# Kernel optimization log

Hardware: AMD Instinct MI355X
Metric: run time of the kernel (lower is better)

The kernel has to match this reference:

```python
import jax, jax.numpy as jnp
import numpy as np

NUM_EMBEDDINGS = 1024
EMBEDDING_DIM = 256


def setup_inputs() -> dict:
    key = jax.random.key(0)
    kx, kc = jax.random.split(key)
    x = jax.random.normal(kx, (32, 256, 64, 64), dtype=jnp.float32)
    # codebook initialized uniform(-1/K, 1/K) as in the torch module
    codebook = jax.random.uniform(
        kc, (NUM_EMBEDDINGS, EMBEDDING_DIM), dtype=jnp.float32,
        minval=-1.0 / NUM_EMBEDDINGS, maxval=1.0 / NUM_EMBEDDINGS)
    return {"x": x, "codebook": codebook}


def reference(x, codebook):
    # x: (B, C, H, W) -> (B, H, W, C) -> (N, C)
    B, C, H, W = x.shape
    xf = jnp.transpose(x, (0, 2, 3, 1)).reshape(-1, C)  # (N, C)
    dist = (jnp.sum(xf * xf, axis=1, keepdims=True)
            + jnp.sum(codebook * codebook, axis=1)
            - 2.0 * jnp.matmul(xf, codebook.T))
    indices = jnp.argmin(dist, axis=1)[:, None]  # (N, 1), matches torch unsqueeze(1)
    quantized = codebook[indices[:, 0]].reshape(B, H, W, C)  # gather
    quantized = jnp.transpose(quantized, (0, 3, 1, 2))  # (B, C, H, W)
    return indices, quantized
```

## Files before the change

### kernel.cpp

```cpp
#include <hip/hip_runtime.h>
#include <stdint.h>

#define CDIM   256
#define KCODES 1024
#define HWSZ   4096
#define NROWS  131072
#define DELTA_P 4.7e-4f

#define WS_BQ    0
#define WS_IDX   4096
#define WS_CBBF  528384
#define WS_CNT   1052672
#define WS_LIST  1052800
#define WS_SLOT  1577216
#define WS_AS    2625792
#define WS_XC    3150080

typedef __attribute__((ext_vector_type(8))) short short8;
typedef __attribute__((ext_vector_type(4))) float f32x4;

__device__ inline unsigned short bf16rne(float f) {
    uint32_t u = __float_as_uint(f);
    u += 0x7FFF + ((u >> 16) & 1);
    return (unsigned short)(u >> 16);
}

__device__ __forceinline__ unsigned umin32(unsigned a, unsigned b) { return a < b ? a : b; }
__device__ __forceinline__ unsigned umax32(unsigned a, unsigned b) { return a > b ? a : b; }

__device__ __forceinline__ unsigned long long packkey(float s, int k) {
    unsigned b = __float_as_uint(s);
    unsigned m = (b & 0x80000000u) ? ~b : (b | 0x80000000u);
    return ((unsigned long long)m << 32) | (unsigned)k;
}

__global__ void codesq_kernel(const float* __restrict__ cb, float* __restrict__ Bq) {
#pragma clang fp contract(off)
    int k = blockIdx.x * 256 + threadIdx.x;
    if (k >= KCODES) return;
    const float* er = cb + (size_t)k * CDIM;
    float half_s[2];
    for (int h = 0; h < 2; ++h) {
        float r[8];
        #pragma unroll
        for (int j = 0; j < 8; ++j) { float v = er[h*128 + j]; r[j] = v * v; }
        for (int i = 8; i < 128; i += 8) {
            #pragma unroll
            for (int j = 0; j < 8; ++j) { float v = er[h*128 + i + j]; float sq = v*v; r[j] = r[j] + sq; }
        }
        half_s[h] = ((r[0]+r[1]) + (r[2]+r[3])) + ((r[4]+r[5]) + (r[6]+r[7]));
    }
    Bq[k] = half_s[0] + half_s[1];
}

__global__ void cbcvt_kernel(const float* __restrict__ cb, unsigned short* __restrict__ cbbf,
                             int* __restrict__ counter) {
    int i = blockIdx.x * 256 + threadIdx.x;
    float4 v = ((const float4*)cb)[i];
    ushort4 o;
    o.x = bf16rne(v.x); o.y = bf16rne(v.y); o.z = bf16rne(v.z); o.w = bf16rne(v.w);
    ((ushort4*)cbbf)[i] = o;
    if (i == 0) *counter = 0;
}

__global__ __launch_bounds__(256, 2)
void screen_kernel(const float* __restrict__ x, const unsigned short* __restrict__ cbbf,
                   const float* __restrict__ Bq,
                   int* __restrict__ idx_out, float* __restrict__ outF,
                   int* __restrict__ flag_list, int* __restrict__ counter,
                   unsigned long long* __restrict__ slots) {
    __shared__ unsigned short xs[64 * 264];
    __shared__ unsigned int sRed[4][64][2];

    const int t = threadIdx.x;
    const int w = t >> 6, l = t & 63;
    const int l15 = l & 15, quad = l >> 4;
    const int r0 = blockIdx.x * 64;
    const float* xbase = x + (size_t)(r0 >> 12) * (CDIM * HWSZ) + (r0 & 4095);

    {
        int cbase = (t >> 4) * 2;
        int row4  = (t & 15) * 4;
        for (int it = 0; it < 8; ++it) {
            int c = cbase + it * 32;
            float4 fa = *(const float4*)(xbase + (size_t)c * HWSZ + row4);
            float4 fb = *(const float4*)(xbase + (size_t)(c + 1) * HWSZ + row4);
            *(uint32_t*)&xs[(row4+0)*264 + c] = (uint32_t)bf16rne(fa.x) | ((uint32_t)bf16rne(fb.x) << 16);
            *(uint32_t*)&xs[(row4+1)*264 + c] = (uint32_t)bf16rne(fa.y) | ((uint32_t)bf16rne(fb.y) << 16);
            *(uint32_t*)&xs[(row4+2)*264 + c] = (uint32_t)bf16rne(fa.z) | ((uint32_t)bf16rne(fb.z) << 16);
            *(uint32_t*)&xs[(row4+3)*264 + c] = (uint32_t)bf16rne(fa.w) | ((uint32_t)bf16rne(fb.w) << 16);
        }
    }

    __syncthreads();

    short8 af[8][4];
    #pragma unroll
    for (int step = 0; step < 8; ++step)
        #pragma unroll
        for (int rf = 0; rf < 4; ++rf)
            af[step][rf] = *(const short8*)&xs[(rf*16 + l15)*264 + step*32 + quad*8];

    const unsigned short* bbase = cbbf + (size_t)(w*32 + l15) * CDIM + quad * 8;
    const int kbase = w*32 + l15;

    unsigned int K1[16], K2[16];
    #pragma unroll
    for (int i = 0; i < 16; ++i) { K1[i] = 0xFFFFFFFFu; K2[i] = 0xFFFFFFFFu; }

    for (int kt = 0; kt < 8; ++kt) {
        float bqp0 = Bq[kt*128 + kbase]      + 0.75f;
        float bqp1 = Bq[kt*128 + kbase + 16] + 0.75f;

        f32x4 acc[4][2];
        #pragma unroll
        for (int rf = 0; rf < 4; ++rf)
            #pragma unroll
            for (int cf = 0; cf < 2; ++cf) acc[rf][cf] = (f32x4){0.f, 0.f, 0.f, 0.f};

        #pragma unroll
        for (int step = 0; step < 8; ++step) {
            int koff = step * 32;
            short8 bfr0 = *(const short8*)(bbase + (size_t)(kt*128)      * CDIM + koff);
            short8 bfr1 = *(const short8*)(bbase + (size_t)(kt*128 + 16) * CDIM + koff);
            #pragma unroll
            for (int rf = 0; rf < 4; ++rf) {
                acc[rf][0] = __builtin_amdgcn_mfma_f32_16x16x32_bf16(af[step][rf], bfr0, acc[rf][0], 0, 0, 0);
                acc[rf][1] = __builtin_amdgcn_mfma_f32_16x16x32_bf16(af[step][rf], bfr1, acc[rf][1], 0, 0, 0);
            }
        }

        unsigned int kk0 = (unsigned)(kt*128 + kbase);
        unsigned int kk1 = kk0 + 16u;
        #pragma unroll
        for (int rf = 0; rf < 4; ++rf)
            #pragma unroll
            for (int reg = 0; reg < 4; ++reg) {
                int st = rf*4 + reg;
                {
                    float s = fmaf(-2.f, acc[rf][0][reg], bqp0);
                    unsigned int key = (__float_as_uint(s) & 0xFFFFFC00u) | kk0;
                    unsigned int t1 = umin32(key, K1[st]);
                    unsigned int t2 = umax32(key, K1[st]);
                    K1[st] = t1;
                    K2[st] = umin32(t2, K2[st]);
                }
                {
                    float s = fmaf(-2.f, acc[rf][1][reg], bqp1);
                    unsigned int key = (__float_as_uint(s) & 0xFFFFFC00u) | kk1;
                    unsigned int t1 = umin32(key, K1[st]);
                    unsigned int t2 = umax32(key, K1[st]);
                    K1[st] = t1;
                    K2[st] = umin32(t2, K2[st]);
                }
            }
    }

    #pragma unroll
    for (int st = 0; st < 16; ++st) {
        #pragma unroll
        for (int m = 1; m < 16; m <<= 1) {
            unsigned int o1 = (unsigned int)__shfl_xor((int)K1[st], m, 64);
            unsigned int o2 = (unsigned int)__shfl_xor((int)K2[st], m, 64);
            unsigned int n2 = umin32(umax32(K1[st], o1), umin32(K2[st], o2));
            K1[st] = umin32(K1[st], o1);
            K2[st] = n2;
        }
    }
    if (l15 == 0) {
        #pragma unroll
        for (int rf = 0; rf < 4; ++rf)
            #pragma unroll
            for (int reg = 0; reg < 4; ++reg) {
                int r = rf*16 + quad*4 + reg;
                int st = rf*4 + reg;
                sRed[w][r][0] = K1[st];
                sRed[w][r][1] = K2[st];
            }
    }
    __syncthreads();
    if (t < 64) {
        unsigned int A1 = sRed[0][t][0], A2 = sRed[0][t][1];
        #pragma unroll
        for (int ww = 1; ww < 4; ++ww) {
            unsigned int B1 = sRed[ww][t][0], B2 = sRed[ww][t][1];
            unsigned int n2 = umin32(umax32(A1, B1), umin32(A2, B2));
            A1 = umin32(A1, B1);
            A2 = n2;
        }
        int row = r0 + t;
        int k1i = (int)(A1 & 1023u);
        idx_out[row] = k1i;
        outF[row] = (float)k1i;
        float v1 = __uint_as_float(A1 & 0xFFFFFC00u);
        float v2 = __uint_as_float(A2 & 0xFFFFFC00u);
        if (!(v2 - v1 > DELTA_P)) {
            int pos = atomicAdd(counter, 1);
            flag_list[pos] = row;
            slots[pos] = 0xFFFFFFFFFFFFFFFFull;
        }
    }
}

__global__ __launch_bounds__(256)
void xcopy_kernel(const float* __restrict__ x, const int* __restrict__ flag_list,
                  const int* __restrict__ counter, float* __restrict__ xc, int capn) {
    int cnt = *counter; if (cnt > capn) cnt = capn;
    for (int base = blockIdx.x * 64; base < cnt; base += gridDim.x * 64) {
        int j = base + (threadIdx.x >> 2);
        if (j < cnt) {
            int row = flag_list[j];
            const float* xr = x + (size_t)(row >> 12) * (CDIM * HWSZ) + (row & 4095);
            int c0 = (threadIdx.x & 3) * 64;
            float* dst = xc + (size_t)j * CDIM + c0;
            #pragma unroll 8
            for (int c = 0; c < 64; ++c)
                dst[c] = xr[(size_t)(c0 + c) * HWSZ];
        }
    }
}

__global__ void asq_kernel(const float* __restrict__ x, const float* __restrict__ xc,
                           const int* __restrict__ flag_list, const int* __restrict__ counter,
                           float* __restrict__ As, int capn) {
#pragma clang fp contract(off)
    int cnt = *counter;
    int jf = blockIdx.x * 256 + threadIdx.x;
    if (jf >= cnt) return;
    const float* src;
    size_t stride;
    if (jf < capn) { src = xc + (size_t)jf * CDIM; stride = 1; }
    else {
        int row = flag_list[jf];
        src = x + (size_t)(row >> 12) * (CDIM * HWSZ) + (row & 4095);
        stride = HWSZ;
    }
    float half_s[2];
    for (int h = 0; h < 2; ++h) {
        float r[8];
        #pragma unroll
        for (int j = 0; j < 8; ++j) { float v = src[(size_t)(h*128 + j) * stride]; r[j] = v * v; }
        for (int i = 8; i < 128; i += 8) {
            #pragma unroll
            for (int j = 0; j < 8; ++j) { float v = src[(size_t)(h*128 + i + j) * stride]; float sq = v*v; r[j] = r[j] + sq; }
        }
        half_s[h] = ((r[0]+r[1]) + (r[2]+r[3])) + ((r[4]+r[5]) + (r[6]+r[7]));
    }
    As[jf] = half_s[0] + half_s[1];
}

__global__ __launch_bounds__(256, 2)
void rescore_kernel(const float* __restrict__ x, const float* __restrict__ cb,
                    const float* __restrict__ Bq,
                    const int* __restrict__ flag_list, const int* __restrict__ counter,
                    const float* __restrict__ xc, const float* __restrict__ As, int capn,
                    unsigned long long* __restrict__ slots) {
    __shared__ float cbs[64 * 256];

    int cnt = *counter;
    if (cnt <= 0) return;
    int nbat  = (cnt + 63) >> 6;
    int nwork = nbat << 4;
    for (int wk = blockIdx.x; wk < nwork; wk += gridDim.x) {
        int bat = wk >> 4;
        int kt0 = (wk & 15) << 6;
        __syncthreads();
        {
            int kc = threadIdx.x >> 2, seg = threadIdx.x & 3;
            const float* crow = cb + (size_t)(kt0 + kc) * CDIM + seg * 64;
            float* dst = &cbs[kc * 256];
            int kw = kc & 7;
            #pragma unroll
            for (int i2 = 0; i2 < 16; ++i2) {
                int lc = seg*16 + i2;
                *(float4*)&dst[(lc ^ kw) << 2] = *(const float4*)&crow[i2 << 2];
            }
        }
        __syncthreads();

        const int rq = threadIdx.x >> 4;
        const int cq = threadIdx.x & 15;
        const int sw = cq & 7;
        const int j0 = bat * 64 + rq * 4;

        int jc[4]; float Ar[4];
        #pragma unroll
        for (int i = 0; i < 4; ++i) {
            int jj = j0 + i;
            jc[i] = (jj < cnt) ? jj : (cnt - 1);
            Ar[i] = As[jc[i]];
        }
        float bq[4]; const float* eb[4];
        #pragma unroll
        for (int j = 0; j < 4; ++j) {
            bq[j] = Bq[kt0 + cq + j*16];
            eb[j] = &cbs[(cq + j*16) * 256];
        }

        float acc[4][4];
        #pragma unroll
        for (int i = 0; i < 4; ++i)
            #pragma unroll
            for (int j = 0; j < 4; ++j) acc[i][j] = 0.f;

        if (jc[3] < capn) {
            const float* xb[4];
            #pragma unroll
            for (int i = 0; i < 4; ++i) xb[i] = xc + (size_t)jc[i] * CDIM;
            #pragma unroll 2
            for (int c4 = 0; c4 < 64; ++c4) {
                float4 ev[4], xv[4];
                #pragma unroll
                for (int j = 0; j < 4; ++j) ev[j] = *(const float4*)&eb[j][(c4 ^ sw) << 2];
                #pragma unroll
                for (int i = 0; i < 4; ++i) xv[i] = *(const float4*)&xb[i][c4 << 2];
                #pragma unroll
                for (int i = 0; i < 4; ++i)
                    #pragma unroll
                    for (int j = 0; j < 4; ++j) {
                        float a = acc[i][j];
                        a = fmaf(xv[i].x, ev[j].x, a);
                        a = fmaf(xv[i].y, ev[j].y, a);
                        a = fmaf(xv[i].z, ev[j].z, a);
                        a = fmaf(xv[i].w, ev[j].w, a);
                        acc[i][j] = a;
                    }
            }
        } else {
            const float* xb[4];
            #pragma unroll
            for (int i = 0; i < 4; ++i) {
                int row = flag_list[jc[i]];
                xb[i] = x + (size_t)(row >> 12) * (CDIM * HWSZ) + (row & 4095);
            }
            for (int c4 = 0; c4 < 64; ++c4) {
                float4 ev[4], xv[4];
                #pragma unroll
                for (int j = 0; j < 4; ++j) ev[j] = *(const float4*)&eb[j][(c4 ^ sw) << 2];
                #pragma unroll
                for (int i = 0; i < 4; ++i) {
                    xv[i].x = xb[i][(size_t)(c4*4 + 0) * HWSZ];
                    xv[i].y = xb[i][(size_t)(c4*4 + 1) * HWSZ];
                    xv[i].z = xb[i][(size_t)(c4*4 + 2) * HWSZ];
                    xv[i].w = xb[i][(size_t)(c4*4 + 3) * HWSZ];
                }
                #pragma unroll
                for (int i = 0; i < 4; ++i)
                    #pragma unroll
                    for (int j = 0; j < 4; ++j) {
                        float a = acc[i][j];
                        a = fmaf(xv[i].x, ev[j].x, a);
                        a = fmaf(xv[i].y, ev[j].y, a);
                        a = fmaf(xv[i].z, ev[j].z, a);
                        a = fmaf(xv[i].w, ev[j].w, a);
                        acc[i][j] = a;
                    }
            }
        }

        float bv[4]; int bk[4];
        #pragma unroll
        for (int i = 0; i < 4; ++i) { bv[i] = 3.4e38f; bk[i] = 0; }
        #pragma unroll
        for (int j = 0; j < 4; ++j) {
            int k = kt0 + cq + j*16;
            #pragma unroll
            for (int i = 0; i < 4; ++i) {
                float T1 = Ar[i] + bq[j];
                float s  = T1 - 2.0f * acc[i][j];
                if (s < bv[i]) { bv[i] = s; bk[i] = k; }
            }
        }
        #pragma unroll
        for (int i = 0; i < 4; ++i) {
            float b = bv[i]; int k = bk[i];
            #pragma unroll
            for (int m = 1; m < 16; m <<= 1) {
                float ov = __shfl_xor(b, m, 64);
                int   ok = __shfl_xor(k, m, 64);
                if (ov < b || (ov == b && ok < k)) { b = ov; k = ok; }
            }
            bv[i] = b; bk[i] = k;
        }
        if (cq == 0) {
            #pragma unroll
            for (int i = 0; i < 4; ++i) {
                int jj = j0 + i;
                if (jj < cnt) atomicMin(&slots[jj], packkey(bv[i], bk[i]));
            }
        }
    }
}

__global__ void fixup_kernel(const unsigned long long* __restrict__ slots,
                             const int* __restrict__ flag_list,
                             const int* __restrict__ counter,
                             int* __restrict__ idx_out, float* __restrict__ outF) {
    int cnt = *counter;
    int t = blockIdx.x * 256 + threadIdx.x;
    if (t >= cnt) return;
    int row = flag_list[t];
    int k = (int)(unsigned)(slots[t] & 0xFFFFFFFFull);
    idx_out[row] = k;
    outF[row] = (float)k;
}

__global__ __launch_bounds__(256)
void gather_kernel(const float* __restrict__ cb, const int* __restrict__ idx,
                   float* __restrict__ out) {
    __shared__ int   sIdx[64];
    __shared__ float tile[64 * 129];
    const int t  = threadIdx.x;
    const int bh = blockIdx.x;
    const int b  = bh >> 6, h = bh & 63;

    if (t < 64) {
        int id = idx[bh * 64 + t];
        sIdx[t] = id;
        out[bh * 64 + t] = (float)id;
    }
    __syncthreads();

    float* qout = out + NROWS + (size_t)b * (CDIM * HWSZ) + h * 64;

    for (int c0 = 0; c0 < CDIM; c0 += 128) {
        if (c0) __syncthreads();
        {
            int ww = t >> 2, seg = t & 3;
            const float* crow = cb + (size_t)sIdx[ww] * CDIM + c0;
            #pragma unroll
            for (int jj = 0; jj < 8; ++jj) {
                int f = seg + 4 * jj;
                float4 v = *(const float4*)(crow + 4 * f);
                float* dst = &tile[ww * 129 + 4 * f];
                dst[0] = v.x; dst[1] = v.y; dst[2] = v.z; dst[3] = v.w;
            }
        }
        __syncthreads();
        {
            int g = t >> 4, w4 = (t & 15) * 4;
            #pragma unroll
            for (int it = 0; it < 8; ++it) {
                int cl = it * 16 + g;
                float4 v;
                v.x = tile[(w4 + 0) * 129 + cl];
                v.y = tile[(w4 + 1) * 129 + cl];
                v.z = tile[(w4 + 2) * 129 + cl];
                v.w = tile[(w4 + 3) * 129 + cl];
                *(float4*)(qout + (size_t)(c0 + cl) * HWSZ + w4) = v;
            }
        }
    }
}

extern "C" void kernel_launch(void* const* d_in, const int* in_sizes, int n_in,
                              void* d_out, int out_size, void* d_ws, size_t ws_size,
                              hipStream_t stream) {
    const float* x  = (const float*)d_in[0];
    const float* cb = (const float*)d_in[1];
    char* ws = (char*)d_ws;
    float*              Bq    = (float*)(ws + WS_BQ);
    int*                idxbf = (int*)(ws + WS_IDX);
    unsigned short*     cbbf  = (unsigned short*)(ws + WS_CBBF);
    int*                cnt   = (int*)(ws + WS_CNT);
    int*                list  = (int*)(ws + WS_LIST);
    unsigned long long* slots = (unsigned long long*)(ws + WS_SLOT);
    float*              As    = (float*)(ws + WS_AS);
    float*              xc    = (float*)(ws + WS_XC);
    float*              out   = (float*)d_out;

    int capn = 0;
    if (ws_size > (size_t)WS_XC) {
        size_t avail = (ws_size - (size_t)WS_XC) / (CDIM * sizeof(float));
        capn = (avail > (size_t)NROWS) ? NROWS : (int)avail;
    }

    codesq_kernel<<<KCODES / 256, 256, 0, stream>>>(cb, Bq);
    cbcvt_kernel <<<256, 256, 0, stream>>>(cb, cbbf, cnt);
    screen_kernel<<<NROWS / 64, 256, 0, stream>>>(x, cbbf, Bq, idxbf, out, list, cnt, slots);
    if (capn > 0)
        xcopy_kernel<<<2048, 256, 0, stream>>>(x, list, cnt, xc, capn);
    asq_kernel   <<<NROWS / 256, 256, 0, stream>>>(x, xc, list, cnt, As, capn);
    rescore_kernel<<<2048, 256, 0, stream>>>(x, cb, Bq, list, cnt, xc, As, capn, slots);
    fixup_kernel <<<NROWS / 256, 256, 0, stream>>>(slots, list, cnt, idxbf, out);
    gather_kernel<<<32 * 64, 256, 0, stream>>>(cb, idxbf, out);
}
```

Baseline: 541.6 us.

## Stream A fragments from LDS per MFMA instead of holding them in registers

The x-tile A fragments (32 short8 per lane) were previously held in registers for the whole codebook sweep. They are now reloaded from LDS on each MFMA. The codebook B fragments for one 16-code column block are preloaded up front, and the two column blocks are processed one after another. This cuts register pressure so more waves can be resident, at the cost of much more LDS read traffic and fewer independent accumulators per inner loop.

```diff
diff --git a/kernel.cpp b/kernel.cpp
--- a/kernel.cpp
+++ b/kernel.cpp
@@ -94,13 +94,6 @@
 
     __syncthreads();
 
-    short8 af[8][4];
-    #pragma unroll
-    for (int step = 0; step < 8; ++step)
-        #pragma unroll
-        for (int rf = 0; rf < 4; ++rf)
-            af[step][rf] = *(const short8*)&xs[(rf*16 + l15)*264 + step*32 + quad*8];
-
     const unsigned short* bbase = cbbf + (size_t)(w*32 + l15) * CDIM + quad * 8;
     const int kbase = w*32 + l15;
 
@@ -109,51 +102,43 @@
     for (int i = 0; i < 16; ++i) { K1[i] = 0xFFFFFFFFu; K2[i] = 0xFFFFFFFFu; }
 
     for (int kt = 0; kt < 8; ++kt) {
-        float bqp0 = Bq[kt*128 + kbase]      + 0.75f;
-        float bqp1 = Bq[kt*128 + kbase + 16] + 0.75f;
-
-        f32x4 acc[4][2];
-        #pragma unroll
-        for (int rf = 0; rf < 4; ++rf)
-            #pragma unroll
-            for (int cf = 0; cf < 2; ++cf) acc[rf][cf] = (f32x4){0.f, 0.f, 0.f, 0.f};
-
-        #pragma unroll
-        for (int step = 0; step < 8; ++step) {
-            int koff = step * 32;
-            short8 bfr0 = *(const short8*)(bbase + (size_t)(kt*128)      * CDIM + koff);
-            short8 bfr1 = *(const short8*)(bbase + (size_t)(kt*128 + 16) * CDIM + koff);
-            #pragma unroll
-            for (int rf = 0; rf < 4; ++rf) {
-                acc[rf][0] = __builtin_amdgcn_mfma_f32_16x16x32_bf16(af[step][rf], bfr0, acc[rf][0], 0, 0, 0);
-                acc[rf][1] = __builtin_amdgcn_mfma_f32_16x16x32_bf16(af[step][rf], bfr1, acc[rf][1], 0, 0, 0);
-            }
-        }
-
-        unsigned int kk0 = (unsigned)(kt*128 + kbase);
-        unsigned int kk1 = kk0 + 16u;
-        #pragma unroll
-        for (int rf = 0; rf < 4; ++rf)
-            #pragma unroll
-            for (int reg = 0; reg < 4; ++reg) {
-                int st = rf*4 + reg;
-                {
-                    float s = fmaf(-2.f, acc[rf][0][reg], bqp0);
-                    unsigned int key = (__float_as_uint(s) & 0xFFFFFC00u) | kk0;
+        #pragma unroll
+        for (int cf = 0; cf < 2; ++cf) {
+            const unsigned short* bb = bbase + (size_t)(kt*128 + cf*16) * CDIM;
+            short8 bfr[8];
+            #pragma unroll
+            for (int step = 0; step < 8; ++step)
+                bfr[step] = *(const short8*)(bb + step * 32);
+
+            float bqp = Bq[kt*128 + kbase + cf*16] + 0.75f;
+
+            f32x4 acc[4];
+            #pragma unroll
+            for (int rf = 0; rf < 4; ++rf) acc[rf] = (f32x4){0.f, 0.f, 0.f, 0.f};
+
+            #pragma unroll
+            for (int step = 0; step < 8; ++step) {
+                #pragma unroll
+                for (int rf = 0; rf < 4; ++rf) {
+                    short8 af = *(const short8*)&xs[(rf*16 + l15)*264 + step*32 + quad*8];
+                    acc[rf] = __builtin_amdgcn_mfma_f32_16x16x32_bf16(af, bfr[step], acc[rf], 0, 0, 0);
+                }
+            }
+
+            unsigned int kk = (unsigned)(kt*128 + kbase + cf*16);
+            #pragma unroll
+            for (int rf = 0; rf < 4; ++rf)
+                #pragma unroll
+                for (int reg = 0; reg < 4; ++reg) {
+                    int st = rf*4 + reg;
+                    float s = fmaf(-2.f, acc[rf][reg], bqp);
+                    unsigned int key = (__float_as_uint(s) & 0xFFFFFC00u) | kk;
                     unsigned int t1 = umin32(key, K1[st]);
                     unsigned int t2 = umax32(key, K1[st]);
                     K1[st] = t1;
                     K2[st] = umin32(t2, K2[st]);
                 }
-                {
-                    float s = fmaf(-2.f, acc[rf][1][reg], bqp1);
-                    unsigned int key = (__float_as_uint(s) & 0xFFFFFC00u) | kk1;
-                    unsigned int t1 = umin32(key, K1[st]);
-                    unsigned int t2 = umax32(key, K1[st]);
-                    K1[st] = t1;
-                    K2[st] = umin32(t2, K2[st]);
-                }
-            }
+        }
     }
 
     #pragma unroll
```

Result: no change. 540.4 us (-0.2%).
